# Performance work log

Hardware: AMD Instinct MI355X
Metric: run time of the kernel (lower is better)

The kernel has to match this reference:

```python
import jax, jax.numpy as jnp
import numpy as np

HID = 128


def _mlp(f, W1, b1, W2, b2, W3, b3):
    h = jax.nn.relu(f @ W1 + b1)
    h = jax.nn.relu(h @ W2 + b2)
    return h @ W3 + b3


def setup_inputs() -> dict:
    key = jax.random.key(0)
    ks = jax.random.split(key, 20)
    B, T = 4096, 256
    x = jax.random.normal(ks[0], (B, T + 1, 2), dtype=jnp.float32)
    t = jax.random.uniform(ks[1], (B, 1), dtype=jnp.float32)

    def lin(k, fan_in, fan_out):
        return jax.random.normal(k, (fan_in, fan_out), jnp.float32) / jnp.sqrt(jnp.float32(fan_in))

    inp = {"x": x, "t": t}
    # forward_score MLP: input = [x_i(2), t(1), x_prev(2), n(1), path_t(2)] = 8
    inp["fw_W1"], inp["fw_b1"] = lin(ks[2], 8, HID), jnp.zeros((HID,), jnp.float32)
    inp["fw_W2"], inp["fw_b2"] = lin(ks[3], HID, HID), jnp.zeros((HID,), jnp.float32)
    inp["fw_W3"], inp["fw_b3"] = lin(ks[4], HID, 2), jnp.zeros((2,), jnp.float32)
    # backward_score MLP: input = [x_i(2), t(1), x_next(2), n(1), path_t(2)] = 8
    inp["bw_W1"], inp["bw_b1"] = lin(ks[5], 8, HID), jnp.zeros((HID,), jnp.float32)
    inp["bw_W2"], inp["bw_b2"] = lin(ks[6], HID, HID), jnp.zeros((HID,), jnp.float32)
    inp["bw_W3"], inp["bw_b3"] = lin(ks[7], HID, 2), jnp.zeros((2,), jnp.float32)
    # initial_score MLP: input = [x_0(2), t(1)] = 3
    inp["in_W1"], inp["in_b1"] = lin(ks[8], 3, HID), jnp.zeros((HID,), jnp.float32)
    inp["in_W2"], inp["in_b2"] = lin(ks[9], HID, HID), jnp.zeros((HID,), jnp.float32)
    inp["in_W3"], inp["in_b3"] = lin(ks[10], HID, 2), jnp.zeros((2,), jnp.float32)
    return inp


def reference(x, t,
              fw_W1, fw_b1, fw_W2, fw_b2, fw_W3, fw_b3,
              bw_W1, bw_b1, bw_W2, bw_b2, bw_W3, bw_b3,
              in_W1, in_b1, in_W2, in_b2, in_W3, in_b3):
    # x: [B, T+1, 2]; last slot is path_t. Equivalent of NeuralNet.get_score,
    # with the per-timestep Python loop batched across the time dimension.
    B = x.shape[0]
    T = x.shape[1] - 1  # ts_len
    x_n = x[:, :-1]                     # [B, T, 2]
    path_t = x[:, -1]                   # [B, 2]

    t_b = jnp.broadcast_to(t[:, None, :], (B, T - 1, 1))        # [B, T-1, 1]
    pt_b = jnp.broadcast_to(path_t[:, None, :], (B, T - 1, 2))  # [B, T-1, 2]

    # forward_score applied at i = 1..T-1, neighbor = x[:, i-1], n = i/T
    n_fwd = (jnp.arange(1, T, dtype=jnp.float32) / T)[None, :, None]
    n_fwd = jnp.broadcast_to(n_fwd, (B, T - 1, 1))
    fwd_feat = jnp.concatenate([x_n[:, 1:], t_b, x_n[:, :-1], n_fwd, pt_b], axis=-1)  # [B,T-1,8]
    fwd_out = _mlp(fwd_feat, fw_W1, fw_b1, fw_W2, fw_b2, fw_W3, fw_b3)                # [B,T-1,2]

    # backward_score applied at i = 0..T-2, neighbor = x[:, i+1], n = i/T
    n_bwd = (jnp.arange(0, T - 1, dtype=jnp.float32) / T)[None, :, None]
    n_bwd = jnp.broadcast_to(n_bwd, (B, T - 1, 1))
    bwd_feat = jnp.concatenate([x_n[:, :-1], t_b, x_n[:, 1:], n_bwd, pt_b], axis=-1)  # [B,T-1,8]
    bwd_out = _mlp(bwd_feat, bw_W1, bw_b1, bw_W2, bw_b2, bw_W3, bw_b3)                # [B,T-1,2]

    # initial_score at i = 0
    init_feat = jnp.concatenate([x_n[:, 0], t], axis=-1)                               # [B,3]
    init_out = _mlp(init_feat, in_W1, in_b1, in_W2, in_b2, in_W3, in_b3)               # [B,2]

    score = jnp.zeros((B, T, 2), dtype=x.dtype)
    score = score.at[:, 1:].add(fwd_out)
    score = score.at[:, :T - 1].add(bwd_out)
    score = score.at[:, 0].add(init_out)
    return score
```

## Files before the change

kernel.cpp:

```cpp
#include <hip/hip_runtime.h>
#include <stdint.h>

typedef __attribute__((ext_vector_type(8))) short short8;
typedef __attribute__((ext_vector_type(4))) float floatx4;

#define MFMA16(a, b, c) __builtin_amdgcn_mfma_f32_16x16x32_bf16(a, b, c, 0, 0, 0)

__device__ __forceinline__ unsigned pkbf(float lo, float hi) {
    const unsigned a = __builtin_bit_cast(unsigned, lo) + 0x8000u;
    const unsigned b = __builtin_bit_cast(unsigned, hi) + 0x8000u;
    return __builtin_amdgcn_perm(b, a, 0x07060302u);
}
__device__ __forceinline__ unsigned short f2bf(float x) {
    unsigned u = __builtin_bit_cast(unsigned, x);
    u = (u + 0x7fffu + ((u >> 16) & 1u)) >> 16;
    return (unsigned short)u;
}

__device__ __forceinline__ int hphys(int row, int u) {
    return row * 64 + ((((u >> 2) ^ (row & 15)) << 2) | (u & 3));
}

__global__ __launch_bounds__(256)
__attribute__((amdgpu_waves_per_eu(4, 4)))
void NeuralNet_37615323578557_kernel(
        const float* __restrict__ x, const float* __restrict__ t,
        const float* __restrict__ fW1, const float* __restrict__ fb1,
        const float* __restrict__ fW2, const float* __restrict__ fb2,
        const float* __restrict__ fW3, const float* __restrict__ fb3,
        const float* __restrict__ gW1, const float* __restrict__ gb1,
        const float* __restrict__ gW2, const float* __restrict__ gb2,
        const float* __restrict__ gW3, const float* __restrict__ gb3,
        const float* __restrict__ iW1, const float* __restrict__ ib1,
        const float* __restrict__ iW2, const float* __restrict__ ib2,
        const float* __restrict__ iW3, const float* __restrict__ ib3,
        float* __restrict__ out) {
    __shared__ unsigned sbuf[8192];
    __shared__ unsigned short fbuf[64 * 8];
    __shared__ float accT[2 * 256 * 2];
    __shared__ unsigned short w3img[256];

    unsigned* const h1buf = sbuf;
    unsigned* const h2buf = sbuf + 4096;

    const int tid  = threadIdx.x;
    const int lane = tid & 63;
    const int w    = tid >> 6;
    const int c    = lane & 15;
    const int q    = lane >> 4;
    const int b0   = blockIdx.x * 2;

    #pragma unroll
    for (int k = 0; k < 4; ++k) accT[tid + k * 256] = 0.0f;
    __syncthreads();

    if (w < 2) {
        float* h1s = (float*)fbuf + w * 128;
        const int b = b0 + w;
        const float* xb = x + (size_t)b * 514;
        const float f0 = xb[0], f1 = xb[1], f2 = t[b];
        const int u0 = lane, u1 = lane + 64;
        const float h0 = fmaxf(iW1[u0] * f0 + iW1[128 + u0] * f1 + iW1[256 + u0] * f2 + ib1[u0], 0.f);
        const float h1 = fmaxf(iW1[u1] * f0 + iW1[128 + u1] * f1 + iW1[256 + u1] * f2 + ib1[u1], 0.f);
        h1s[u0] = h0;
        h1s[u1] = h1;
        float a0 = ib2[lane], a1 = ib2[lane + 64];
        for (int k = 0; k < 128; ++k) {
            const float hv = h1s[k];
            a0 += hv * iW2[k * 128 + lane];
            a1 += hv * iW2[k * 128 + lane + 64];
        }
        a0 = fmaxf(a0, 0.f); a1 = fmaxf(a1, 0.f);
        float p0 = a0 * iW3[lane * 2 + 0] + a1 * iW3[(lane + 64) * 2 + 0];
        float p1 = a0 * iW3[lane * 2 + 1] + a1 * iW3[(lane + 64) * 2 + 1];
        #pragma unroll
        for (int m = 1; m < 64; m <<= 1) {
            p0 += __shfl_xor(p0, m, 64);
            p1 += __shfl_xor(p1, m, 64);
        }
        if (lane == 0) {
            accT[w * 512 + 0] += p0 + ib3[0];
            accT[w * 512 + 1] += p1 + ib3[1];
        }
    }

    const int wbase = w * 32;
    const int ucol  = w * 16 + c;

    for (int dir = 0; dir < 2; ++dir) {
        const float* W1 = dir ? gW1 : fW1;
        const float* B1 = dir ? gb1 : fb1;
        const float* W2 = dir ? gW2 : fW2;
        const float* B2 = dir ? gb2 : fb2;
        const float* W3 = dir ? gW3 : fW3;
        const float* B3 = dir ? gb3 : fb3;
        const int posoff = (1 - dir) * 2;

        __syncthreads();

        {
            const int k0  = (tid & 63) << 1;
            const int c0  = (tid >> 6) << 5;
            const int rot = (tid >> 2) & 15;
            const int ks  = k0 >> 5;
            const int q2  = (k0 >> 3) & 3;
            const int j0  = k0 & 7;
            const float* r0p = &W2[k0 * 128 + c0];
            const float* r1p = r0p + 128;
            const int usb = (q2 << 4) * 8 + j0;
            #pragma unroll 4
            for (int nn2 = 0; nn2 < 16; ++nn2) {
                const int off = ((nn2 + rot) & 15) << 1;
                const float2 v0 = *(const float2*)(r0p + off);
                const float2 v1 = *(const float2*)(r1p + off);
                #pragma unroll
                for (int e = 0; e < 2; ++e) {
                    const int n = c0 + off + e;
                    const unsigned pv = pkbf(e ? v0.y : v0.x, e ? v1.y : v1.x);
                    const int B = ((n >> 5) * 2 + (n & 1)) * 4 + ks;
                    const int us = B * 512 + ((n >> 1) & 15) * 8 + usb;
                    sbuf[us >> 1] = pv;
                }
            }
        }

        if (tid < 128) {
            const int ks3 = tid >> 5, q3 = (tid >> 3) & 3;
            const int c3 = (tid >> 2) & 1, jp = tid & 3;
            const int k = ks3 * 32 + q3 * 8 + jp * 2;
            ((unsigned*)w3img)[tid] = pkbf(W3[k * 2 + c3], W3[(k + 1) * 2 + c3]);
        }

        short8 w1f[2];
        float  b1v[2], b2v[2];
        #pragma unroll
        for (int ntl = 0; ntl < 2; ++ntl) {
            const int col = wbase + 2 * c + ntl;
            b1v[ntl] = B1[col];
            b2v[ntl] = B2[col];
            short8 f = {0, 0, 0, 0, 0, 0, 0, 0};
            if (q == 0) {
                #pragma unroll
                for (int j = 0; j < 8; ++j) f[j] = (short)f2bf(W1[j * 128 + col]);
            }
            w1f[ntl] = f;
        }
        const float b3c = (c < 2) ? B3[c] : 0.0f;
        __syncthreads();

        short8 w2f[2][4];
        {
            const unsigned short* img = (const unsigned short*)sbuf;
            #pragma unroll
            for (int ntl = 0; ntl < 2; ++ntl)
                #pragma unroll
                for (int ks = 0; ks < 4; ++ks)
                    w2f[ntl][ks] = *(const short8*)
                        &img[(((w * 2 + ntl) * 4 + ks) << 9) + lane * 8];
        }

        #pragma unroll 1
        for (int tt = 0; tt < 8; ++tt) {
            const int r0 = tt * 64;

            if (tid < 64) {
                const int r = r0 + tid;
                unsigned v0 = 0, v1 = 0, v2 = 0, v3 = 0;
                if (r < 510) {
                    const int bl = (r >= 255) ? 1 : 0;
                    const int i  = r - bl * 255;
                    const float* xb = x + (size_t)(b0 + bl) * 514;
                    const float2 xi  = *(const float2*)(xb + 2 * i);
                    const float2 xi1 = *(const float2*)(xb + 2 * i + 2);
                    const float2 pt  = *(const float2*)(xb + 512);
                    const float tv = t[b0 + bl];
                    const float nv = (float)(dir ? i : (i + 1)) * (1.0f / 256.0f);
                    if (dir == 0) {
                        v0 = pkbf(xi1.x, xi1.y);
                        v1 = pkbf(tv, xi.x);
                        v2 = pkbf(xi.y, nv);
                    } else {
                        v0 = pkbf(xi.x, xi.y);
                        v1 = pkbf(tv, xi1.x);
                        v2 = pkbf(xi1.y, nv);
                    }
                    v3 = pkbf(pt.x, pt.y);
                }
                unsigned* fp = (unsigned*)&fbuf[tid * 8];
                fp[0] = v0; fp[1] = v1; fp[2] = v2; fp[3] = v3;
            }
            __syncthreads();

            #pragma unroll
            for (int mt = 0; mt < 4; ++mt) {
                short8 af = {0, 0, 0, 0, 0, 0, 0, 0};
                if (q == 0) af = *(const short8*)&fbuf[(mt * 16 + c) * 8];
                floatx4 a0 = {b1v[0], b1v[0], b1v[0], b1v[0]};
                floatx4 a1 = {b1v[1], b1v[1], b1v[1], b1v[1]};
                a0 = MFMA16(af, w1f[0], a0);
                a1 = MFMA16(af, w1f[1], a1);
                const int rowb = mt * 16 + q * 4;
                #pragma unroll
                for (int rr = 0; rr < 4; ++rr)
                    h1buf[hphys(rowb + rr, ucol)] =
                        pkbf(fmaxf(a0[rr], 0.0f), fmaxf(a1[rr], 0.0f));
            }
            __syncthreads();

            #pragma unroll
            for (int mt = 0; mt < 4; ++mt) {
                const unsigned* rp = &h1buf[(mt * 16 + c) * 64];
                const int base = (q ^ c) << 2;
                short8 a0 = *(const short8*)&rp[base];
                short8 a1 = *(const short8*)&rp[base ^ 16];
                short8 a2 = *(const short8*)&rp[base ^ 32];
                short8 a3 = *(const short8*)&rp[base ^ 48];
                floatx4 s0 = {b2v[0], b2v[0], b2v[0], b2v[0]};
                floatx4 s1 = {b2v[1], b2v[1], b2v[1], b2v[1]};
                s0 = MFMA16(a0, w2f[0][0], s0); s1 = MFMA16(a0, w2f[1][0], s1);
                s0 = MFMA16(a1, w2f[0][1], s0); s1 = MFMA16(a1, w2f[1][1], s1);
                s0 = MFMA16(a2, w2f[0][2], s0); s1 = MFMA16(a2, w2f[1][2], s1);
                s0 = MFMA16(a3, w2f[0][3], s0); s1 = MFMA16(a3, w2f[1][3], s1);
                const int rowb = mt * 16 + q * 4;
                #pragma unroll
                for (int rr = 0; rr < 4; ++rr)
                    h2buf[hphys(rowb + rr, ucol)] =
                        pkbf(fmaxf(s0[rr], 0.0f), fmaxf(s1[rr], 0.0f));
            }
            __syncthreads();

            {
                const unsigned* rp = &h2buf[(w * 16 + c) * 64];
                const int base = (q ^ c) << 2;
                short8 a0 = *(const short8*)&rp[base];
                short8 a1 = *(const short8*)&rp[base ^ 16];
                short8 a2 = *(const short8*)&rp[base ^ 32];
                short8 a3 = *(const short8*)&rp[base ^ 48];
                const unsigned short* w3p = w3img + ((q * 2 + (c & 1)) << 3);
                floatx4 s = {b3c, b3c, b3c, b3c};
                s = MFMA16(a0, *(const short8*)&w3p[0],   s);
                s = MFMA16(a1, *(const short8*)&w3p[64],  s);
                s = MFMA16(a2, *(const short8*)&w3p[128], s);
                s = MFMA16(a3, *(const short8*)&w3p[192], s);
                if (c < 2) {
                    const int rb = r0 + w * 16 + q * 4;
                    #pragma unroll
                    for (int rr = 0; rr < 4; ++rr) {
                        const int r = rb + rr;
                        if (r < 510) {
                            const int idx = 2 * r + ((r >= 255) ? 2 : 0)
                                          + posoff + c;
                            atomicAdd(&accT[idx], s[rr]);
                        }
                    }
                }
            }
        }
    }

    __syncthreads();
    ((float4*)(out + (size_t)b0 * 512))[tid] = ((const float4*)accT)[tid];
}

extern "C" void kernel_launch(void* const* d_in, const int* in_sizes, int n_in,
                              void* d_out, int out_size, void* d_ws, size_t ws_size,
                              hipStream_t stream) {
    (void)in_sizes; (void)n_in; (void)d_ws; (void)ws_size; (void)out_size;
    const float* x   = (const float*)d_in[0];
    const float* t   = (const float*)d_in[1];
    const float* fW1 = (const float*)d_in[2];
    const float* fb1 = (const float*)d_in[3];
    const float* fW2 = (const float*)d_in[4];
    const float* fb2 = (const float*)d_in[5];
    const float* fW3 = (const float*)d_in[6];
    const float* fb3 = (const float*)d_in[7];
    const float* gW1 = (const float*)d_in[8];
    const float* gb1 = (const float*)d_in[9];
    const float* gW2 = (const float*)d_in[10];
    const float* gb2 = (const float*)d_in[11];
    const float* gW3 = (const float*)d_in[12];
    const float* gb3 = (const float*)d_in[13];
    const float* iW1 = (const float*)d_in[14];
    const float* ib1 = (const float*)d_in[15];
    const float* iW2 = (const float*)d_in[16];
    const float* ib2 = (const float*)d_in[17];
    const float* iW3 = (const float*)d_in[18];
    const float* ib3 = (const float*)d_in[19];
    float* out = (float*)d_out;

    NeuralNet_37615323578557_kernel<<<dim3(2048), 256, 0, stream>>>(
        x, t, fW1, fb1, fW2, fb2, fW3, fb3,
        gW1, gb1, gW2, gb2, gW3, gb3,
        iW1, ib1, iW2, ib2, iW3, ib3, out);
}
```

Before: 261.7 us.

## Split block into two wave-pairs processing alternate row tiles independently

The four waves are regrouped into two pairs, each pair handling its own 32-row tile with separate h1/h2 LDS buffers. Within a pair each wave covers 64 hidden columns, so it holds twice as many W2 fragments in registers (16 short8 instead of 8). The W2 image is staged in two halves through LDS with extra barriers. This is meant to halve the rows per step and raise per-wave MFMA work between syncs, but it raises register pressure, and the occupancy hint is loosened to 3-4 waves per EU to allow for that.

```diff
diff --git a/kernel.cpp b/kernel.cpp
--- a/kernel.cpp
+++ b/kernel.cpp
@@ -22,7 +22,7 @@
 }
 
 __global__ __launch_bounds__(256)
-__attribute__((amdgpu_waves_per_eu(4, 4)))
+__attribute__((amdgpu_waves_per_eu(3, 4)))
 void NeuralNet_37615323578557_kernel(
         const float* __restrict__ x, const float* __restrict__ t,
         const float* __restrict__ fW1, const float* __restrict__ fb1,
@@ -36,19 +36,21 @@
         const float* __restrict__ iW3, const float* __restrict__ ib3,
         float* __restrict__ out) {
     __shared__ unsigned sbuf[8192];
-    __shared__ unsigned short fbuf[64 * 8];
+    __shared__ unsigned short fbuf[2 * 256];
     __shared__ float accT[2 * 256 * 2];
     __shared__ unsigned short w3img[256];
-
-    unsigned* const h1buf = sbuf;
-    unsigned* const h2buf = sbuf + 4096;
 
     const int tid  = threadIdx.x;
     const int lane = tid & 63;
     const int w    = tid >> 6;
+    const int p    = w >> 1;
+    const int v    = w & 1;
     const int c    = lane & 15;
     const int q    = lane >> 4;
     const int b0   = blockIdx.x * 2;
+
+    unsigned* const hp1 = sbuf + p * 4096;
+    unsigned* const hp2 = sbuf + p * 4096 + 2048;
 
     #pragma unroll
     for (int k = 0; k < 4; ++k) accT[tid + k * 256] = 0.0f;
@@ -84,9 +86,6 @@
         }
     }
 
-    const int wbase = w * 32;
-    const int ucol  = w * 16 + c;
-
     for (int dir = 0; dir < 2; ++dir) {
         const float* W1 = dir ? gW1 : fW1;
         const float* B1 = dir ? gb1 : fb1;
@@ -98,44 +97,60 @@
 
         __syncthreads();
 
+        short8 w2f[4][4];
         {
             const int k0  = (tid & 63) << 1;
-            const int c0  = (tid >> 6) << 5;
-            const int rot = (tid >> 2) & 15;
+            const int rot = (tid >> 2) & 7;
             const int ks  = k0 >> 5;
             const int q2  = (k0 >> 3) & 3;
             const int j0  = k0 & 7;
-            const float* r0p = &W2[k0 * 128 + c0];
-            const float* r1p = r0p + 128;
             const int usb = (q2 << 4) * 8 + j0;
-            #pragma unroll 4
-            for (int nn2 = 0; nn2 < 16; ++nn2) {
-                const int off = ((nn2 + rot) & 15) << 1;
-                const float2 v0 = *(const float2*)(r0p + off);
-                const float2 v1 = *(const float2*)(r1p + off);
-                #pragma unroll
-                for (int e = 0; e < 2; ++e) {
-                    const int n = c0 + off + e;
-                    const unsigned pv = pkbf(e ? v0.y : v0.x, e ? v1.y : v1.x);
-                    const int B = ((n >> 5) * 2 + (n & 1)) * 4 + ks;
-                    const int us = B * 512 + ((n >> 1) & 15) * 8 + usb;
-                    sbuf[us >> 1] = pv;
-                }
-            }
-        }
-
-        if (tid < 128) {
-            const int ks3 = tid >> 5, q3 = (tid >> 3) & 3;
-            const int c3 = (tid >> 2) & 1, jp = tid & 3;
-            const int k = ks3 * 32 + q3 * 8 + jp * 2;
-            ((unsigned*)w3img)[tid] = pkbf(W3[k * 2 + c3], W3[(k + 1) * 2 + c3]);
-        }
-
-        short8 w1f[2];
-        float  b1v[2], b2v[2];
+            const int cg  = (tid >> 6) << 4;
+
+            #pragma unroll
+            for (int half = 0; half < 2; ++half) {
+                const int c0 = half * 64 + cg;
+                const float* r0p = &W2[k0 * 128 + c0];
+                const float* r1p = r0p + 128;
+                #pragma unroll 4
+                for (int nn2 = 0; nn2 < 8; ++nn2) {
+                    const int off = ((nn2 + rot) & 7) << 1;
+                    const float2 v0 = *(const float2*)(r0p + off);
+                    const float2 v1 = *(const float2*)(r1p + off);
+                    #pragma unroll
+                    for (int e = 0; e < 2; ++e) {
+                        const int n = c0 + off + e;
+                        const unsigned pv = pkbf(e ? v0.y : v0.x, e ? v1.y : v1.x);
+                        const int B = (((n >> 5) * 2 + (n & 1)) * 4 + ks) - half * 16;
+                        const int us = B * 512 + ((n >> 1) & 15) * 8 + usb;
+                        sbuf[us >> 1] = pv;
+                    }
+                }
+                if (half == 0 && tid < 128) {
+                    const int ks3 = tid >> 5, q3 = (tid >> 3) & 3;
+                    const int c3 = (tid >> 2) & 1, jp = tid & 3;
+                    const int k = ks3 * 32 + q3 * 8 + jp * 2;
+                    ((unsigned*)w3img)[tid] = pkbf(W3[k * 2 + c3], W3[(k + 1) * 2 + c3]);
+                }
+                __syncthreads();
+                if (v == half) {
+                    const unsigned short* img = (const unsigned short*)sbuf;
+                    #pragma unroll
+                    for (int ntl = 0; ntl < 4; ++ntl)
+                        #pragma unroll
+                        for (int kss = 0; kss < 4; ++kss)
+                            w2f[ntl][kss] = *(const short8*)
+                                &img[((ntl * 4 + kss) << 9) + lane * 8];
+                }
+                __syncthreads();
+            }
+        }
+
+        short8 w1f[4];
+        float  b1v[4], b2v[4];
         #pragma unroll
-        for (int ntl = 0; ntl < 2; ++ntl) {
-            const int col = wbase + 2 * c + ntl;
+        for (int ntl = 0; ntl < 4; ++ntl) {
+            const int col = (v << 6) + ((ntl >> 1) << 5) + 2 * c + (ntl & 1);
             b1v[ntl] = B1[col];
             b2v[ntl] = B2[col];
             short8 f = {0, 0, 0, 0, 0, 0, 0, 0};
@@ -146,26 +161,15 @@
             w1f[ntl] = f;
         }
         const float b3c = (c < 2) ? B3[c] : 0.0f;
-        __syncthreads();
-
-        short8 w2f[2][4];
-        {
-            const unsigned short* img = (const unsigned short*)sbuf;
-            #pragma unroll
-            for (int ntl = 0; ntl < 2; ++ntl)
-                #pragma unroll
-                for (int ks = 0; ks < 4; ++ks)
-                    w2f[ntl][ks] = *(const short8*)
-                        &img[(((w * 2 + ntl) * 4 + ks) << 9) + lane * 8];
-        }
 
         #pragma unroll 1
-        for (int tt = 0; tt < 8; ++tt) {
-            const int r0 = tt * 64;
-
-            if (tid < 64) {
-                const int r = r0 + tid;
-                unsigned v0 = 0, v1 = 0, v2 = 0, v3 = 0;
+        for (int s = 0; s < 8; ++s) {
+            const int tt = (s << 1) | p;
+            const int r0 = tt * 32;
+
+            if (v == 0 && lane < 32) {
+                const int r = r0 + lane;
+                unsigned f0 = 0, f1 = 0, f2 = 0, f3 = 0;
                 if (r < 510) {
                     const int bl = (r >= 255) ? 1 : 0;
                     const int i  = r - bl * 255;
@@ -176,40 +180,48 @@
                     const float tv = t[b0 + bl];
                     const float nv = (float)(dir ? i : (i + 1)) * (1.0f / 256.0f);
                     if (dir == 0) {
-                        v0 = pkbf(xi1.x, xi1.y);
-                        v1 = pkbf(tv, xi.x);
-                        v2 = pkbf(xi.y, nv);
+                        f0 = pkbf(xi1.x, xi1.y);
+                        f1 = pkbf(tv, xi.x);
+                        f2 = pkbf(xi.y, nv);
                     } else {
-                        v0 = pkbf(xi.x, xi.y);
-                        v1 = pkbf(tv, xi1.x);
-                        v2 = pkbf(xi1.y, nv);
+                        f0 = pkbf(xi.x, xi.y);
+                        f1 = pkbf(tv, xi1.x);
+                        f2 = pkbf(xi1.y, nv);
                     }
-                    v3 = pkbf(pt.x, pt.y);
-                }
-                unsigned* fp = (unsigned*)&fbuf[tid * 8];
-                fp[0] = v0; fp[1] = v1; fp[2] = v2; fp[3] = v3;
+                    f3 = pkbf(pt.x, pt.y);
+                }
+                unsigned* fp = (unsigned*)&fbuf[p * 256 + lane * 8];
+                fp[0] = f0; fp[1] = f1; fp[2] = f2; fp[3] = f3;
             }
             __syncthreads();
 
             #pragma unroll
-            for (int mt = 0; mt < 4; ++mt) {
+            for (int mt = 0; mt < 2; ++mt) {
                 short8 af = {0, 0, 0, 0, 0, 0, 0, 0};
-                if (q == 0) af = *(const short8*)&fbuf[(mt * 16 + c) * 8];
+                if (q == 0)
+                    af = *(const short8*)&fbuf[p * 256 + (mt * 16 + c) * 8];
                 floatx4 a0 = {b1v[0], b1v[0], b1v[0], b1v[0]};
                 floatx4 a1 = {b1v[1], b1v[1], b1v[1], b1v[1]};
+                floatx4 a2 = {b1v[2], b1v[2], b1v[2], b1v[2]};
+                floatx4 a3 = {b1v[3], b1v[3], b1v[3], b1v[3]};
                 a0 = MFMA16(af, w1f[0], a0);
                 a1 = MFMA16(af, w1f[1], a1);
+                a2 = MFMA16(af, w1f[2], a2);
+                a3 = MFMA16(af, w1f[3], a3);
                 const int rowb = mt * 16 + q * 4;
                 #pragma unroll
-                for (int rr = 0; rr < 4; ++rr)
-                    h1buf[hphys(rowb + rr, ucol)] =
+                for (int rr = 0; rr < 4; ++rr) {
+                    hp1[hphys(rowb + rr, (v << 5) + c)] =
                         pkbf(fmaxf(a0[rr], 0.0f), fmaxf(a1[rr], 0.0f));
+                    hp1[hphys(rowb + rr, (v << 5) + 16 + c)] =
+                        pkbf(fmaxf(a2[rr], 0.0f), fmaxf(a3[rr], 0.0f));
+                }
             }
             __syncthreads();
 
             #pragma unroll
-            for (int mt = 0; mt < 4; ++mt) {
-                const unsigned* rp = &h1buf[(mt * 16 + c) * 64];
+            for (int mt = 0; mt < 2; ++mt) {
+                const unsigned* rp = &hp1[(mt * 16 + c) * 64];
                 const int base = (q ^ c) << 2;
                 short8 a0 = *(const short8*)&rp[base];
                 short8 a1 = *(const short8*)&rp[base ^ 16];
@@ -217,40 +229,50 @@
                 short8 a3 = *(const short8*)&rp[base ^ 48];
                 floatx4 s0 = {b2v[0], b2v[0], b2v[0], b2v[0]};
                 floatx4 s1 = {b2v[1], b2v[1], b2v[1], b2v[1]};
+                floatx4 s2 = {b2v[2], b2v[2], b2v[2], b2v[2]};
+                floatx4 s3 = {b2v[3], b2v[3], b2v[3], b2v[3]};
                 s0 = MFMA16(a0, w2f[0][0], s0); s1 = MFMA16(a0, w2f[1][0], s1);
+                s2 = MFMA16(a0, w2f[2][0], s2); s3 = MFMA16(a0, w2f[3][0], s3);
                 s0 = MFMA16(a1, w2f[0][1], s0); s1 = MFMA16(a1, w2f[1][1], s1);
+                s2 = MFMA16(a1, w2f[2][1], s2); s3 = MFMA16(a1, w2f[3][1], s3);
                 s0 = MFMA16(a2, w2f[0][2], s0); s1 = MFMA16(a2, w2f[1][2], s1);
+                s2 = MFMA16(a2, w2f[2][2], s2); s3 = MFMA16(a2, w2f[3][2], s3);
                 s0 = MFMA16(a3, w2f[0][3], s0); s1 = MFMA16(a3, w2f[1][3], s1);
+                s2 = MFMA16(a3, w2f[2][3], s2); s3 = MFMA16(a3, w2f[3][3], s3);
                 const int rowb = mt * 16 + q * 4;
                 #pragma unroll
-                for (int rr = 0; rr < 4; ++rr)
-                    h2buf[hphys(rowb + rr, ucol)] =
+                for (int rr = 0; rr < 4; ++rr) {
+                    hp2[hphys(rowb + rr, (v << 5) + c)] =
                         pkbf(fmaxf(s0[rr], 0.0f), fmaxf(s1[rr], 0.0f));
+                    hp2[hphys(rowb + rr, (v << 5) + 16 + c)] =
+                        pkbf(fmaxf(s2[rr], 0.0f), fmaxf(s3[rr], 0.0f));
+                }
             }
             __syncthreads();
 
             {
-                const unsigned* rp = &h2buf[(w * 16 + c) * 64];
+                const unsigned short* w3p = w3img + ((q * 2 + (c & 1)) << 3);
+                const int rowblk = v << 4;
+                const unsigned* rp = &hp2[(rowblk + c) * 64];
                 const int base = (q ^ c) << 2;
                 short8 a0 = *(const short8*)&rp[base];
                 short8 a1 = *(const short8*)&rp[base ^ 16];
                 short8 a2 = *(const short8*)&rp[base ^ 32];
                 short8 a3 = *(const short8*)&rp[base ^ 48];
-                const unsigned short* w3p = w3img + ((q * 2 + (c & 1)) << 3);
-                floatx4 s = {b3c, b3c, b3c, b3c};
-                s = MFMA16(a0, *(const short8*)&w3p[0],   s);
-                s = MFMA16(a1, *(const short8*)&w3p[64],  s);
-                s = MFMA16(a2, *(const short8*)&w3p[128], s);
-                s = MFMA16(a3, *(const short8*)&w3p[192], s);
+                floatx4 ss = {b3c, b3c, b3c, b3c};
+                ss = MFMA16(a0, *(const short8*)&w3p[0],   ss);
+                ss = MFMA16(a1, *(const short8*)&w3p[64],  ss);
+                ss = MFMA16(a2, *(const short8*)&w3p[128], ss);
+                ss = MFMA16(a3, *(const short8*)&w3p[192], ss);
                 if (c < 2) {
-                    const int rb = r0 + w * 16 + q * 4;
+                    const int rb = r0 + rowblk + q * 4;
                     #pragma unroll
                     for (int rr = 0; rr < 4; ++rr) {
                         const int r = rb + rr;
                         if (r < 510) {
                             const int idx = 2 * r + ((r >= 255) ? 2 : 0)
                                           + posoff + c;
-                            atomicAdd(&accT[idx], s[rr]);
+                            atomicAdd(&accT[idx], ss[rr]);
                         }
                     }
                 }
```

Result: slower. 821.2 us (+213.8%).
